# Kernel optimization log

Measured on AMD Instinct MI355X. Metric: run time of the kernel, lower is better.

Reference implementation:

```python
import jax, jax.numpy as jnp
import numpy as np
import math

B, S, D, H = 2048, 32, 1024, 16
DK = D // H
EPS = 1e-5

def setup_inputs() -> dict:
    key = jax.random.key(0)
    ks = jax.random.split(key, 8)
    w_scale = 0.02  # realistic init scale for linear weights
    # Weights stored as (d_in, d_out): y = x @ W + b (same math as torch x @ W.T)
    return {
        "x":  jax.random.normal(ks[0], (B, S, D), jnp.float32),
        "ln_g": jnp.ones((D,), jnp.float32),
        "ln_b": jnp.zeros((D,), jnp.float32),
        "wq": jax.random.normal(ks[1], (D, D), jnp.float32) * w_scale,
        "bq": jnp.zeros((D,), jnp.float32),
        "wk": jax.random.normal(ks[2], (D, D), jnp.float32) * w_scale,
        "bk": jnp.zeros((D,), jnp.float32),
        "wv": jax.random.normal(ks[3], (D, D), jnp.float32) * w_scale,
        "bv": jnp.zeros((D,), jnp.float32),
        "wo": jax.random.normal(ks[4], (D, D), jnp.float32) * w_scale,
        "bo": jnp.zeros((D,), jnp.float32),
        "rel_bias": jax.random.normal(ks[5], (H, 32, 32), jnp.float32),
    }

def reference(x, ln_g, ln_b, wq, bq, wk, bk, wv, bv, wo, bo, rel_bias):
    b, s, d = x.shape
    h = rel_bias.shape[0]
    dk = d // h
    residual = x
    # LayerNorm (eps=1e-5)
    mu = jnp.mean(x, axis=-1, keepdims=True)
    var = jnp.mean(jnp.square(x - mu), axis=-1, keepdims=True)
    xn = (x - mu) * jax.lax.rsqrt(var + EPS) * ln_g + ln_b
    # QKV projections -> [b, h, s, dk]
    def split_heads(t):
        return t.reshape(b, s, h, dk).transpose(0, 2, 1, 3)
    Q = split_heads(xn @ wq + bq)
    K = split_heads(xn @ wk + bk)
    V = split_heads(xn @ wv + bv)
    scores = jnp.einsum('bhqd,bhkd->bhqk', Q, K) / jnp.sqrt(jnp.float32(dk))
    if s <= 32:  # static at trace time, matching the torch branch
        scores = scores + rel_bias[:, :s, :s][None]
    attn = jax.nn.softmax(scores, axis=-1)
    ctx = jnp.einsum('bhqk,bhkd->bhqd', attn, V)
    ctx = ctx.transpose(0, 2, 1, 3).reshape(b, s, d)
    out = ctx @ wo + bo  # dropout is identity in eval
    return residual + out
```

## Files before the change

### kernel.cpp

```cpp
#include <hip/hip_runtime.h>
#include <stdint.h>


typedef __attribute__((ext_vector_type(8))) short bf16x8;
typedef __attribute__((ext_vector_type(4))) float f32x4;
typedef __attribute__((ext_vector_type(16))) float f32x16;

__device__ __forceinline__ float bf2f(unsigned short u) {
    return __uint_as_float(((unsigned)u) << 16);
}
__device__ __forceinline__ unsigned short f2bf(float f) {
    unsigned u = __float_as_uint(f);
    u += 0x7FFFu + ((u >> 16) & 1u);
    return (unsigned short)(u >> 16);
}
__device__ __forceinline__ uint4 pack8(const float* f) {
    uint4 u;
    u.x = (unsigned)f2bf(f[0]) | ((unsigned)f2bf(f[1]) << 16);
    u.y = (unsigned)f2bf(f[2]) | ((unsigned)f2bf(f[3]) << 16);
    u.z = (unsigned)f2bf(f[4]) | ((unsigned)f2bf(f[5]) << 16);
    u.w = (unsigned)f2bf(f[6]) | ((unsigned)f2bf(f[7]) << 16);
    return u;
}

typedef __attribute__((address_space(3))) unsigned lds_u32;
typedef const __attribute__((address_space(1))) unsigned glb_u32;
__device__ __forceinline__ void gld16(const void* g, void* l) {
    __builtin_amdgcn_global_load_lds((glb_u32*)g, (lds_u32*)l, 16, 0, 0);
}

__global__ __launch_bounds__(256) void transpose_w(
    const float* __restrict__ wq, const float* __restrict__ wk,
    const float* __restrict__ wv, const float* __restrict__ wo,
    unsigned short* __restrict__ wcatT, unsigned short* __restrict__ woT)
{
    __shared__ unsigned short T[64 * 72];
    int bid = blockIdx.x;
    int p = bid >> 8;
    int t = bid & 255;
    int k0 = (t >> 4) * 64, n0 = (t & 15) * 64;
    const float* src = (p == 0) ? wq : (p == 1) ? wk : (p == 2) ? wv : wo;
    unsigned short* dst = (p < 3) ? (wcatT + (size_t)p * 1048576) : woT;
    int tid = threadIdx.x;
#pragma unroll
    for (int it = 0; it < 2; it++) {
        int flat = it * 2048 + tid * 8;
        int r = flat >> 6, c = flat & 63;
        const float* s4 = src + (size_t)(k0 + r) * 1024 + n0 + c;
        float4 u0 = *(const float4*)s4;
        float4 u1 = *(const float4*)(s4 + 4);
        float f[8] = {u0.x, u0.y, u0.z, u0.w, u1.x, u1.y, u1.z, u1.w};
        *(uint4*)&T[r * 72 + c] = pack8(f);
    }
    __syncthreads();
#pragma unroll
    for (int it = 0; it < 2; it++) {
        int flat = it * 2048 + tid * 8;
        int rn = flat >> 6, ck = flat & 63;
        unsigned short v[8];
#pragma unroll
        for (int j = 0; j < 8; j++) v[j] = T[(ck + j) * 72 + rn];
        uint4 u;
        u.x = (unsigned)v[0] | ((unsigned)v[1] << 16);
        u.y = (unsigned)v[2] | ((unsigned)v[3] << 16);
        u.z = (unsigned)v[4] | ((unsigned)v[5] << 16);
        u.w = (unsigned)v[6] | ((unsigned)v[7] << 16);
        *(uint4*)(dst + (size_t)(n0 + rn) * 1024 + k0 + ck) = u;
    }
}

__global__ __launch_bounds__(256) void ln_kernel(
    const float* __restrict__ x, const float* __restrict__ gg,
    const float* __restrict__ bb, unsigned short* __restrict__ xn)
{
    int l = threadIdx.x & 63;
    size_t row = (size_t)blockIdx.x * 4 + (threadIdx.x >> 6);
    const float* xr = x + row * 1024;
    float f0[8], f1[8];
    *(float4*)&f0[0] = *(const float4*)(xr + l * 8);
    *(float4*)&f0[4] = *(const float4*)(xr + l * 8 + 4);
    *(float4*)&f1[0] = *(const float4*)(xr + 512 + l * 8);
    *(float4*)&f1[4] = *(const float4*)(xr + 512 + l * 8 + 4);
    float s = 0.f, s2 = 0.f;
#pragma unroll
    for (int j = 0; j < 8; j++) { s += f0[j] + f1[j]; s2 += f0[j] * f0[j] + f1[j] * f1[j]; }
#pragma unroll
    for (int m = 1; m < 64; m <<= 1) { s += __shfl_xor(s, m); s2 += __shfl_xor(s2, m); }
    float mu = s * (1.f / 1024.f);
    float var = s2 * (1.f / 1024.f) - mu * mu;
    float rs = rsqrtf(var + 1e-5f);
    float fg0[8], fg1[8], fb0[8], fb1[8];
    *(float4*)&fg0[0] = *(const float4*)(gg + l * 8);
    *(float4*)&fg0[4] = *(const float4*)(gg + l * 8 + 4);
    *(float4*)&fg1[0] = *(const float4*)(gg + 512 + l * 8);
    *(float4*)&fg1[4] = *(const float4*)(gg + 512 + l * 8 + 4);
    *(float4*)&fb0[0] = *(const float4*)(bb + l * 8);
    *(float4*)&fb0[4] = *(const float4*)(bb + l * 8 + 4);
    *(float4*)&fb1[0] = *(const float4*)(bb + 512 + l * 8);
    *(float4*)&fb1[4] = *(const float4*)(bb + 512 + l * 8 + 4);
    float o0[8], o1[8];
#pragma unroll
    for (int j = 0; j < 8; j++) {
        o0[j] = (f0[j] - mu) * rs * fg0[j] + fb0[j];
        o1[j] = (f1[j] - mu) * rs * fg1[j] + fb1[j];
    }
    *(uint4*)(xn + row * 1024 + l * 8) = pack8(o0);
    *(uint4*)(xn + row * 1024 + 512 + l * 8) = pack8(o1);
}

#define FENCE asm volatile("" ::: "memory")
#define BARRIER do { FENCE; __builtin_amdgcn_s_barrier(); FENCE; } while (0)
#define WAIT_LGKM0 do { asm volatile("s_waitcnt lgkmcnt(0)" ::: "memory"); \
                        __builtin_amdgcn_sched_barrier(0); } while (0)
#define VMCNT(n) asm volatile("s_waitcnt vmcnt(" #n ")" ::: "memory")

#define FQ_SA(buf) (LDSU + (buf) * 16384)
#define FQ_SB(buf) (LDSU + 32768 + (buf) * 12288)
#define QS_OFF 0
#define KS_OFF 18432
#define VT_OFF 36864
#define PS_OFF 57344

#define ASTG(buf, g, koff) gld16(Ag + (size_t)(g) * 65536 + (koff), FQ_SA(buf) + ((g) * 64 + w * 8) * 64)
#define BSTG(buf, p, koff) gld16(((p) == 0 ? Bgq : (p) == 1 ? Bgk : Bgv) + (koff), \
                                 FQ_SB(buf) + ((p) * 64 + w * 8) * 64)

#define FLDA(buf, q, rfq, ks) (*(const bf16x8*)&FQ_SA(buf)[ \
    (wm * 128 + (q) * 32 + (rfq) * 16 + (l & 15)) * 64 + ((((ks) * 32) + khi) ^ aswz)])
#define FLDB(buf, cf, ks) (*(const bf16x8*)&FQ_SB(buf)[ \
    (wn * 48 + (cf) * 16 + (l & 15)) * 64 + ((((ks) * 32) + khi) ^ aswz)])

#define MFMA_TRI(q) do { \
    _Pragma("unroll") \
    for (int cf = 0; cf < 3; cf++) { \
        acc[(q)*2+0][cf] = __builtin_amdgcn_mfma_f32_16x16x32_bf16(aF00, bF[cf][0], acc[(q)*2+0][cf], 0, 0, 0); \
        acc[(q)*2+0][cf] = __builtin_amdgcn_mfma_f32_16x16x32_bf16(aF01, bF[cf][1], acc[(q)*2+0][cf], 0, 0, 0); \
        acc[(q)*2+1][cf] = __builtin_amdgcn_mfma_f32_16x16x32_bf16(aF10, bF[cf][0], acc[(q)*2+1][cf], 0, 0, 0); \
        acc[(q)*2+1][cf] = __builtin_amdgcn_mfma_f32_16x16x32_bf16(aF11, bF[cf][1], acc[(q)*2+1][cf], 0, 0, 0); \
    } } while (0)

#define FPHASE(buf, q, STAGE_STMT, TAIL_STMT) do { \
    bf16x8 aF00 = FLDA(buf, q, 0, 0), aF01 = FLDA(buf, q, 0, 1); \
    bf16x8 aF10 = FLDA(buf, q, 1, 0), aF11 = FLDA(buf, q, 1, 1); \
    if ((q) == 0) { \
        _Pragma("unroll") \
        for (int cf = 0; cf < 3; cf++) { bF[cf][0] = FLDB(buf, cf, 0); bF[cf][1] = FLDB(buf, cf, 1); } \
    } \
    STAGE_STMT; \
    BARRIER; \
    WAIT_LGKM0; \
    __builtin_amdgcn_s_setprio(1); \
    MFMA_TRI(q); \
    __builtin_amdgcn_s_setprio(0); \
    TAIL_STMT; \
    BARRIER; \
} while (0)

__global__ __launch_bounds__(512, 1) void fqa_kernel(
    const unsigned short* __restrict__ A, const unsigned short* __restrict__ wcatT,
    const float* __restrict__ bq, const float* __restrict__ bk,
    const float* __restrict__ bv, const float* __restrict__ rb,
    unsigned short* __restrict__ ctx)
{
    __shared__ __align__(16) unsigned short LDSU[67584];
    int cpx = gridDim.x >> 3;
    int bid = (blockIdx.x & 7) * cpx + (blockIdx.x >> 3);
    int mp = bid >> 4, h = bid & 15;
    int m0 = mp * 256;
    int tid = threadIdx.x, l = tid & 63, w = tid >> 6;
    int wm = w >> 2, wn = w & 3;
    int khi = (l >> 4) * 8;
    int aswz = (l & 7) * 8;
    int swzc = ((l & 7) ^ (l >> 3)) * 8;

    const unsigned short* Ag  = A + (size_t)(m0 + w * 8 + (l >> 3)) * 1024 + swzc;
    const unsigned short* Bgq = wcatT + (size_t)(h * 64 + w * 8 + (l >> 3)) * 1024 + swzc;
    const unsigned short* Bgk = Bgq + 1048576ull;
    const unsigned short* Bgv = Bgq + 2097152ull;

    f32x4 acc[8][3];
#pragma unroll
    for (int i = 0; i < 8; i++)
#pragma unroll
        for (int j = 0; j < 3; j++)
#pragma unroll
            for (int v = 0; v < 4; v++) acc[i][j][v] = 0.f;

    bf16x8 bF[3][2];

    ASTG(0, 0, 0); ASTG(0, 1, 0); ASTG(0, 2, 0); ASTG(0, 3, 0);
    BSTG(0, 0, 0); BSTG(0, 1, 0); BSTG(0, 2, 0);
    BSTG(1, 0, 64); BSTG(1, 1, 64); BSTG(1, 2, 64);
    VMCNT(3);
    BARRIER;

    for (int it = 0; it < 7; ++it) {
        int ko1 = (2 * it + 1) * 64, ko2 = (2 * it + 2) * 64, ko3 = (2 * it + 3) * 64;
        FPHASE(0, 0, do { ASTG(1, 0, ko1); ASTG(1, 1, ko1); } while (0), (void)0);
        FPHASE(0, 1, do { ASTG(1, 2, ko1); ASTG(1, 3, ko1); } while (0), (void)0);
        FPHASE(0, 2, do { BSTG(0, 0, ko2); BSTG(0, 1, ko2); } while (0), (void)0);
        FPHASE(0, 3, BSTG(0, 2, ko2), VMCNT(3));
        FPHASE(1, 0, do { ASTG(0, 0, ko2); ASTG(0, 1, ko2); } while (0), (void)0);
        FPHASE(1, 1, do { ASTG(0, 2, ko2); ASTG(0, 3, ko2); } while (0), (void)0);
        FPHASE(1, 2, do { BSTG(1, 0, ko3); BSTG(1, 1, ko3); } while (0), (void)0);
        FPHASE(1, 3, BSTG(1, 2, ko3), VMCNT(3));
    }
    FPHASE(0, 0, do { ASTG(1, 0, 960); ASTG(1, 1, 960); } while (0), (void)0);
    FPHASE(0, 1, do { ASTG(1, 2, 960); ASTG(1, 3, 960); } while (0), (void)0);
    FPHASE(0, 2, (void)0, (void)0);
    FPHASE(0, 3, (void)0, VMCNT(0));
    FPHASE(1, 0, (void)0, (void)0);
    FPHASE(1, 1, (void)0, (void)0);
    FPHASE(1, 2, (void)0, (void)0);
    FPHASE(1, 3, (void)0, (void)0);
    __builtin_amdgcn_sched_barrier(0);

#pragma unroll
    for (int cf = 0; cf < 3; cf++) {
        int seg = (wn * 3 + cf) >> 2;
        int cseg = wn * 48 + cf * 16 + (l & 15) - (seg << 6);
        const float* bp = (seg == 0) ? bq : (seg == 1) ? bk : bv;
        float bias = bp[h * 64 + cseg];
#pragma unroll
        for (int ai = 0; ai < 8; ai++) {
#pragma unroll
            for (int v = 0; v < 4; v++) {
                int row = wm * 128 + ai * 16 + (l >> 4) * 4 + v;
                unsigned short val = f2bf(acc[ai][cf][v] + bias);
                if (seg == 0)      LDSU[QS_OFF + row * 72 + cseg] = val;
                else if (seg == 1) LDSU[KS_OFF + row * 72 + cseg] = val;
                else               LDSU[VT_OFF + (((row >> 5) << 6) + cseg) * 40 + (row & 31)] = val;
            }
        }
    }
    __syncthreads();

    {
        int col = l & 31, hi = l >> 5;
        f32x16 s;
#pragma unroll
        for (int i = 0; i < 16; i++) s[i] = 0.f;
#pragma unroll
        for (int t = 0; t < 4; t++) {
            bf16x8 aQ = *(const bf16x8*)&LDSU[QS_OFF + (w * 32 + col) * 72 + t * 16 + hi * 8];
            bf16x8 bK = *(const bf16x8*)&LDSU[KS_OFF + (w * 32 + col) * 72 + t * 16 + hi * 8];
            s = __builtin_amdgcn_mfma_f32_32x32x16_bf16(aQ, bK, s, 0, 0, 0);
        }
        const float* rbh = rb + h * 1024;
        unsigned short* ps = LDSU + PS_OFF + w * 1280;
#pragma unroll
        for (int r = 0; r < 16; r++) {
            int m = (r & 3) + 8 * (r >> 2) + 4 * hi;
            float v = s[r] * 0.125f + rbh[m * 32 + col];
            float mx = v;
#pragma unroll
            for (int msk = 1; msk < 32; msk <<= 1) mx = fmaxf(mx, __shfl_xor(mx, msk));
            float e = __expf(v - mx);
            float sm = e;
#pragma unroll
            for (int msk = 1; msk < 32; msk <<= 1) sm += __shfl_xor(sm, msk);
            ps[m * 40 + col] = f2bf(e / sm);
        }
        bf16x8 pa0 = *(const bf16x8*)&ps[col * 40 + hi * 8];
        bf16x8 pa1 = *(const bf16x8*)&ps[col * 40 + 16 + hi * 8];
        size_t rowb = ((size_t)mp * 8 + w) * 32;
#pragma unroll
        for (int c2 = 0; c2 < 2; c2++) {
            bf16x8 vb0 = *(const bf16x8*)&LDSU[VT_OFF + (w * 64 + c2 * 32 + col) * 40 + hi * 8];
            bf16x8 vb1 = *(const bf16x8*)&LDSU[VT_OFF + (w * 64 + c2 * 32 + col) * 40 + 16 + hi * 8];
            f32x16 o;
#pragma unroll
            for (int i = 0; i < 16; i++) o[i] = 0.f;
            o = __builtin_amdgcn_mfma_f32_32x32x16_bf16(pa0, vb0, o, 0, 0, 0);
            o = __builtin_amdgcn_mfma_f32_32x32x16_bf16(pa1, vb1, o, 0, 0, 0);
#pragma unroll
            for (int r = 0; r < 16; r++) {
                int m = (r & 3) + 8 * (r >> 2) + 4 * hi;
                ctx[(rowb + m) * 1024 + h * 64 + c2 * 32 + col] = f2bf(o[r]);
            }
        }
    }
}

#define SAp(buf) (LDSU + (buf) * 16384)
#define SBp(buf) (LDSU + 32768 + (buf) * 16384)

#define STG(gb, hh, kcol, ldsreg) do { \
    const unsigned short* _g = (gb) + (size_t)((hh) * 128) * 1024 + (kcol); \
    unsigned short* _d = (ldsreg) + ((hh) * 128 + w * 8) * 64; \
    gld16(_g, _d); gld16(_g + 64 * 1024, _d + 64 * 64); } while (0)

#define LDA(buf, q, rfq, ks) (*(const bf16x8*)&SAp(buf)[ \
    (wm * 128 + (q) * 32 + (rfq) * 16 + (l & 15)) * 64 + ((((ks) * 32) + khi) ^ aswz)])
#define LDB(buf, cf, ks) (*(const bf16x8*)&SBp(buf)[ \
    (wn * 64 + (cf) * 16 + (l & 15)) * 64 + ((((ks) * 32) + khi) ^ aswz)])

#define MFMA_QUAD(q) do { \
    _Pragma("unroll") \
    for (int cf = 0; cf < 4; cf++) { \
        acc[(q)*2+0][cf] = __builtin_amdgcn_mfma_f32_16x16x32_bf16(aF00, bF[cf][0], acc[(q)*2+0][cf], 0, 0, 0); \
        acc[(q)*2+0][cf] = __builtin_amdgcn_mfma_f32_16x16x32_bf16(aF01, bF[cf][1], acc[(q)*2+0][cf], 0, 0, 0); \
        acc[(q)*2+1][cf] = __builtin_amdgcn_mfma_f32_16x16x32_bf16(aF10, bF[cf][0], acc[(q)*2+1][cf], 0, 0, 0); \
        acc[(q)*2+1][cf] = __builtin_amdgcn_mfma_f32_16x16x32_bf16(aF11, bF[cf][1], acc[(q)*2+1][cf], 0, 0, 0); \
    } } while (0)

#define PHASE(buf, q, STAGE_STMT, TAIL_STMT) do { \
    bf16x8 aF00 = LDA(buf, q, 0, 0), aF01 = LDA(buf, q, 0, 1); \
    bf16x8 aF10 = LDA(buf, q, 1, 0), aF11 = LDA(buf, q, 1, 1); \
    if ((q) == 0) { \
        _Pragma("unroll") \
        for (int cf = 0; cf < 4; cf++) { bF[cf][0] = LDB(buf, cf, 0); bF[cf][1] = LDB(buf, cf, 1); } \
    } \
    STAGE_STMT; \
    BARRIER; \
    WAIT_LGKM0; \
    __builtin_amdgcn_s_setprio(1); \
    MFMA_QUAD(q); \
    __builtin_amdgcn_s_setprio(0); \
    TAIL_STMT; \
    BARRIER; \
} while (0)

__global__ __launch_bounds__(512, 2) void gemm8res(
    const unsigned short* __restrict__ A, const unsigned short* __restrict__ Bt,
    const float* __restrict__ bz0, const float* __restrict__ resid,
    float* __restrict__ out, int NTL)
{
    __shared__ __align__(16) unsigned short LDSU[65536];
    int cpx = gridDim.x >> 3;
    int bid = (blockIdx.x & 7) * cpx + (blockIdx.x >> 3);
    int mt = bid / NTL, ntl = bid % NTL;
    int m0 = mt * 256, n0 = ntl * 256;
    int tid = threadIdx.x, l = tid & 63, w = tid >> 6;
    int wm = w >> 2, wn = w & 3;
    int khi = (l >> 4) * 8;
    int aswz = (l & 7) * 8;

    const unsigned short* Ag = A + (size_t)(m0 + w * 8 + (l >> 3)) * 1024 + ((l & 7) ^ (l >> 3)) * 8;
    const unsigned short* Bg = Bt + (size_t)(n0 + w * 8 + (l >> 3)) * 1024 + ((l & 7) ^ (l >> 3)) * 8;
    unsigned short* sA0 = SAp(0);
    unsigned short* sA1 = SAp(1);
    unsigned short* sB0 = SBp(0);
    unsigned short* sB1 = SBp(1);

    f32x4 acc[8][4];
#pragma unroll
    for (int i = 0; i < 8; i++)
#pragma unroll
        for (int j = 0; j < 4; j++)
#pragma unroll
            for (int v = 0; v < 4; v++) acc[i][j][v] = 0.f;

    bf16x8 bF[4][2];

    STG(Ag, 0, 0, sA0); STG(Ag, 1, 0, sA0);
    STG(Bg, 0, 0, sB0); STG(Bg, 1, 0, sB0);
    STG(Bg, 0, 64, sB1); STG(Bg, 1, 64, sB1);
    VMCNT(4);
    BARRIER;

    for (int it = 0; it < 7; ++it) {
        int koff = it * 128;
        PHASE(0, 0, STG(Ag, 0, koff + 64, sA1), (void)0);
        PHASE(0, 1, STG(Ag, 1, koff + 64, sA1), (void)0);
        PHASE(0, 2, STG(Bg, 0, koff + 128, sB0), (void)0);
        PHASE(0, 3, STG(Bg, 1, koff + 128, sB0), VMCNT(4));
        PHASE(1, 0, STG(Ag, 0, koff + 128, sA0), (void)0);
        PHASE(1, 1, STG(Ag, 1, koff + 128, sA0), (void)0);
        PHASE(1, 2, STG(Bg, 0, koff + 192, sB1), (void)0);
        PHASE(1, 3, STG(Bg, 1, koff + 192, sB1), VMCNT(4));
    }
    PHASE(0, 0, STG(Ag, 0, 960, sA1), (void)0);
    PHASE(0, 1, STG(Ag, 1, 960, sA1), (void)0);
    PHASE(0, 2, (void)0, (void)0);
    PHASE(0, 3, (void)0, VMCNT(0));
    PHASE(1, 0, (void)0, (void)0);
    PHASE(1, 1, (void)0, (void)0);
    PHASE(1, 2, (void)0, (void)0);
    PHASE(1, 3, (void)0, (void)0);
    __builtin_amdgcn_sched_barrier(0);

    float* Cf = (float*)LDSU;
    int gcol = n0 + l * 4;
    float4 bzv = *(const float4*)(bz0 + gcol);
#pragma unroll
    for (int pass = 0; pass < 2; pass++) {
        __syncthreads();
#pragma unroll
        for (int rfq = 0; rfq < 4; rfq++) {
            int rf = pass * 4 + rfq;
#pragma unroll
            for (int cf = 0; cf < 4; cf++) {
                int c0 = wn * 64 + cf * 16 + (l & 15);
                int c4 = c0 >> 2, ce = c0 & 3;
#pragma unroll
                for (int v = 0; v < 4; v++) {
                    int rl = wm * 64 + rfq * 16 + (l >> 4) * 4 + v;
                    Cf[rl * 256 + ((c4 ^ (rl & 7)) << 2) + ce] = acc[rf][cf][v];
                }
            }
        }
        __syncthreads();
#pragma unroll
        for (int rb4 = 0; rb4 < 4; rb4++) {
            float4 rz[4], cv[4];
#pragma unroll
            for (int k = 0; k < 4; k++) {
                int rr = (rb4 * 4 + k) * 8 + w;
                int grow = m0 + (rr & 63) + ((rr >> 6) << 7) + pass * 64;
                rz[k] = *(const float4*)(resid + (size_t)grow * 1024 + gcol);
            }
#pragma unroll
            for (int k = 0; k < 4; k++) {
                int rr = (rb4 * 4 + k) * 8 + w;
                cv[k] = *(const float4*)&Cf[rr * 256 + ((l ^ (rr & 7)) << 2)];
            }
#pragma unroll
            for (int k = 0; k < 4; k++) {
                int rr = (rb4 * 4 + k) * 8 + w;
                int grow = m0 + (rr & 63) + ((rr >> 6) << 7) + pass * 64;
                float4 o;
                o.x = cv[k].x + bzv.x + rz[k].x;
                o.y = cv[k].y + bzv.y + rz[k].y;
                o.z = cv[k].z + bzv.z + rz[k].z;
                o.w = cv[k].w + bzv.w + rz[k].w;
                *(float4*)(out + (size_t)grow * 1024 + gcol) = o;
            }
        }
    }
}

extern "C" void kernel_launch(void* const* d_in, const int* in_sizes, int n_in,
                              void* d_out, int out_size, void* d_ws, size_t ws_size,
                              hipStream_t stream)
{
    const float* x  = (const float*)d_in[0];
    const float* lg = (const float*)d_in[1];
    const float* lb = (const float*)d_in[2];
    const float* wq = (const float*)d_in[3];
    const float* bq = (const float*)d_in[4];
    const float* wk = (const float*)d_in[5];
    const float* bk = (const float*)d_in[6];
    const float* wv = (const float*)d_in[7];
    const float* bv = (const float*)d_in[8];
    const float* wo = (const float*)d_in[9];
    const float* bo = (const float*)d_in[10];
    const float* rb = (const float*)d_in[11];
    float* out = (float*)d_out;
    unsigned short* ws = (unsigned short*)d_ws;

    unsigned short* wcatT = ws;
    unsigned short* woT   = wcatT + 3145728;
    unsigned short* xn    = woT + 1048576;
    unsigned short* ctx   = xn + 67108864ull;

    transpose_w<<<dim3(1024), dim3(256), 0, stream>>>(wq, wk, wv, wo, wcatT, woT);
    ln_kernel<<<dim3(16384), dim3(256), 0, stream>>>(x, lg, lb, xn);

    fqa_kernel<<<dim3(4096), dim3(512), 0, stream>>>(xn, wcatT, bq, bk, bv, rb, ctx);

    gemm8res<<<dim3(1024), dim3(512), 0, stream>>>(ctx, woT, bo, x, out, 4);
}
```

Baseline: 782.1 us.

## Halve fused QKV-attention tile to 128 rows with 256-thread blocks, two per CU

The fused LN-output x QKV projection plus attention kernel now processes 128 rows per block with 4 waves instead of 256 rows with 8 waves. Each wave computes a 64x96 tile with six column fragments, and LDS drops to about 80KB so two blocks can be resident per CU. The grid doubles to 8192 blocks. The aim is better latency hiding and occupancy, at the cost of reading the weight tiles from global memory twice as often per output row.

After: 777.8 us. About the same (-0.5%).

```diff
diff --git a/kernel.cpp b/kernel.cpp
--- a/kernel.cpp
+++ b/kernel.cpp
@@ -114,61 +114,59 @@
                         __builtin_amdgcn_sched_barrier(0); } while (0)
 #define VMCNT(n) asm volatile("s_waitcnt vmcnt(" #n ")" ::: "memory")
 
-#define FQ_SA(buf) (LDSU + (buf) * 16384)
-#define FQ_SB(buf) (LDSU + 32768 + (buf) * 12288)
+#define FQ_SA(buf) (LDSU + (buf) * 8192)
+#define FQ_SB(buf) (LDSU + 16384 + (buf) * 12288)
 #define QS_OFF 0
-#define KS_OFF 18432
-#define VT_OFF 36864
-#define PS_OFF 57344
-
-#define ASTG(buf, g, koff) gld16(Ag + (size_t)(g) * 65536 + (koff), FQ_SA(buf) + ((g) * 64 + w * 8) * 64)
-#define BSTG(buf, p, koff) gld16(((p) == 0 ? Bgq : (p) == 1 ? Bgk : Bgv) + (koff), \
-                                 FQ_SB(buf) + ((p) * 64 + w * 8) * 64)
-
-#define FLDA(buf, q, rfq, ks) (*(const bf16x8*)&FQ_SA(buf)[ \
-    (wm * 128 + (q) * 32 + (rfq) * 16 + (l & 15)) * 64 + ((((ks) * 32) + khi) ^ aswz)])
+#define KS_OFF 9216
+#define VT_OFF 18432
+#define PS_OFF 28672
+
+#define ASTG(buf, g, koff) gld16(Ag + (size_t)(g) * 32768 + (koff), \
+                                 FQ_SA(buf) + ((g) * 32 + w * 8) * 64)
+#define BSTG(buf, p, c, koff) gld16(((p) == 0 ? Bgq : (p) == 1 ? Bgk : Bgv) + (size_t)(c) * 32768 + (koff), \
+                                    FQ_SB(buf) + ((p) * 64 + (c) * 32 + w * 8) * 64)
+
+#define FLDA(buf, q, ks) (*(const bf16x8*)&FQ_SA(buf)[ \
+    (wm * 64 + (q) * 16 + (l & 15)) * 64 + ((((ks) * 32) + khi) ^ aswz)])
 #define FLDB(buf, cf, ks) (*(const bf16x8*)&FQ_SB(buf)[ \
-    (wn * 48 + (cf) * 16 + (l & 15)) * 64 + ((((ks) * 32) + khi) ^ aswz)])
-
-#define MFMA_TRI(q) do { \
+    (wn * 96 + (cf) * 16 + (l & 15)) * 64 + ((((ks) * 32) + khi) ^ aswz)])
+
+#define MFMA_HEX(q) do { \
     _Pragma("unroll") \
-    for (int cf = 0; cf < 3; cf++) { \
-        acc[(q)*2+0][cf] = __builtin_amdgcn_mfma_f32_16x16x32_bf16(aF00, bF[cf][0], acc[(q)*2+0][cf], 0, 0, 0); \
-        acc[(q)*2+0][cf] = __builtin_amdgcn_mfma_f32_16x16x32_bf16(aF01, bF[cf][1], acc[(q)*2+0][cf], 0, 0, 0); \
-        acc[(q)*2+1][cf] = __builtin_amdgcn_mfma_f32_16x16x32_bf16(aF10, bF[cf][0], acc[(q)*2+1][cf], 0, 0, 0); \
-        acc[(q)*2+1][cf] = __builtin_amdgcn_mfma_f32_16x16x32_bf16(aF11, bF[cf][1], acc[(q)*2+1][cf], 0, 0, 0); \
+    for (int cf = 0; cf < 6; cf++) { \
+        acc[q][cf] = __builtin_amdgcn_mfma_f32_16x16x32_bf16(aF0, bF[cf][0], acc[q][cf], 0, 0, 0); \
+        acc[q][cf] = __builtin_amdgcn_mfma_f32_16x16x32_bf16(aF1, bF[cf][1], acc[q][cf], 0, 0, 0); \
     } } while (0)
 
 #define FPHASE(buf, q, STAGE_STMT, TAIL_STMT) do { \
-    bf16x8 aF00 = FLDA(buf, q, 0, 0), aF01 = FLDA(buf, q, 0, 1); \
-    bf16x8 aF10 = FLDA(buf, q, 1, 0), aF11 = FLDA(buf, q, 1, 1); \
+    bf16x8 aF0 = FLDA(buf, q, 0), aF1 = FLDA(buf, q, 1); \
     if ((q) == 0) { \
         _Pragma("unroll") \
-        for (int cf = 0; cf < 3; cf++) { bF[cf][0] = FLDB(buf, cf, 0); bF[cf][1] = FLDB(buf, cf, 1); } \
+        for (int cf = 0; cf < 6; cf++) { bF[cf][0] = FLDB(buf, cf, 0); bF[cf][1] = FLDB(buf, cf, 1); } \
     } \
     STAGE_STMT; \
     BARRIER; \
     WAIT_LGKM0; \
     __builtin_amdgcn_s_setprio(1); \
-    MFMA_TRI(q); \
+    MFMA_HEX(q); \
     __builtin_amdgcn_s_setprio(0); \
     TAIL_STMT; \
     BARRIER; \
 } while (0)
 
-__global__ __launch_bounds__(512, 1) void fqa_kernel(
+__global__ __launch_bounds__(256, 2) void fqa2_kernel(
     const unsigned short* __restrict__ A, const unsigned short* __restrict__ wcatT,
     const float* __restrict__ bq, const float* __restrict__ bk,
     const float* __restrict__ bv, const float* __restrict__ rb,
     unsigned short* __restrict__ ctx)
 {
-    __shared__ __align__(16) unsigned short LDSU[67584];
+    __shared__ __align__(16) unsigned short LDSU[40960];
     int cpx = gridDim.x >> 3;
     int bid = (blockIdx.x & 7) * cpx + (blockIdx.x >> 3);
     int mp = bid >> 4, h = bid & 15;
-    int m0 = mp * 256;
+    int m0 = mp * 128;
     int tid = threadIdx.x, l = tid & 63, w = tid >> 6;
-    int wm = w >> 2, wn = w & 3;
+    int wm = w >> 1, wn = w & 1;
     int khi = (l >> 4) * 8;
     int aswz = (l & 7) * 8;
     int swzc = ((l & 7) ^ (l >> 3)) * 8;
@@ -178,32 +176,34 @@
     const unsigned short* Bgk = Bgq + 1048576ull;
     const unsigned short* Bgv = Bgq + 2097152ull;
 
-    f32x4 acc[8][3];
-#pragma unroll
-    for (int i = 0; i < 8; i++)
-#pragma unroll
-        for (int j = 0; j < 3; j++)
+    f32x4 acc[4][6];
+#pragma unroll
+    for (int i = 0; i < 4; i++)
+#pragma unroll
+        for (int j = 0; j < 6; j++)
 #pragma unroll
             for (int v = 0; v < 4; v++) acc[i][j][v] = 0.f;
 
-    bf16x8 bF[3][2];
+    bf16x8 bF[6][2];
 
     ASTG(0, 0, 0); ASTG(0, 1, 0); ASTG(0, 2, 0); ASTG(0, 3, 0);
-    BSTG(0, 0, 0); BSTG(0, 1, 0); BSTG(0, 2, 0);
-    BSTG(1, 0, 64); BSTG(1, 1, 64); BSTG(1, 2, 64);
-    VMCNT(3);
+    BSTG(0, 0, 0, 0); BSTG(0, 0, 1, 0); BSTG(0, 1, 0, 0);
+    BSTG(0, 1, 1, 0); BSTG(0, 2, 0, 0); BSTG(0, 2, 1, 0);
+    BSTG(1, 0, 0, 64); BSTG(1, 0, 1, 64); BSTG(1, 1, 0, 64);
+    BSTG(1, 1, 1, 64); BSTG(1, 2, 0, 64); BSTG(1, 2, 1, 64);
+    VMCNT(6);
     BARRIER;
 
     for (int it = 0; it < 7; ++it) {
         int ko1 = (2 * it + 1) * 64, ko2 = (2 * it + 2) * 64, ko3 = (2 * it + 3) * 64;
         FPHASE(0, 0, do { ASTG(1, 0, ko1); ASTG(1, 1, ko1); } while (0), (void)0);
         FPHASE(0, 1, do { ASTG(1, 2, ko1); ASTG(1, 3, ko1); } while (0), (void)0);
-        FPHASE(0, 2, do { BSTG(0, 0, ko2); BSTG(0, 1, ko2); } while (0), (void)0);
-        FPHASE(0, 3, BSTG(0, 2, ko2), VMCNT(3));
+        FPHASE(0, 2, do { BSTG(0, 0, 0, ko2); BSTG(0, 0, 1, ko2); BSTG(0, 1, 0, ko2); } while (0), (void)0);
+        FPHASE(0, 3, do { BSTG(0, 1, 1, ko2); BSTG(0, 2, 0, ko2); BSTG(0, 2, 1, ko2); } while (0), VMCNT(6));
         FPHASE(1, 0, do { ASTG(0, 0, ko2); ASTG(0, 1, ko2); } while (0), (void)0);
         FPHASE(1, 1, do { ASTG(0, 2, ko2); ASTG(0, 3, ko2); } while (0), (void)0);
-        FPHASE(1, 2, do { BSTG(1, 0, ko3); BSTG(1, 1, ko3); } while (0), (void)0);
-        FPHASE(1, 3, BSTG(1, 2, ko3), VMCNT(3));
+        FPHASE(1, 2, do { BSTG(1, 0, 0, ko3); BSTG(1, 0, 1, ko3); BSTG(1, 1, 0, ko3); } while (0), (void)0);
+        FPHASE(1, 3, do { BSTG(1, 1, 1, ko3); BSTG(1, 2, 0, ko3); BSTG(1, 2, 1, ko3); } while (0), VMCNT(6));
     }
     FPHASE(0, 0, do { ASTG(1, 0, 960); ASTG(1, 1, 960); } while (0), (void)0);
     FPHASE(0, 1, do { ASTG(1, 2, 960); ASTG(1, 3, 960); } while (0), (void)0);
@@ -216,16 +216,17 @@
     __builtin_amdgcn_sched_barrier(0);
 
 #pragma unroll
-    for (int cf = 0; cf < 3; cf++) {
-        int seg = (wn * 3 + cf) >> 2;
-        int cseg = wn * 48 + cf * 16 + (l & 15) - (seg << 6);
+    for (int cf = 0; cf < 6; cf++) {
+        int colg = wn * 96 + cf * 16 + (l & 15);
+        int seg = colg >> 6;
+        int cseg = colg & 63;
         const float* bp = (seg == 0) ? bq : (seg == 1) ? bk : bv;
         float bias = bp[h * 64 + cseg];
 #pragma unroll
-        for (int ai = 0; ai < 8; ai++) {
+        for (int ai = 0; ai < 4; ai++) {
 #pragma unroll
             for (int v = 0; v < 4; v++) {
-                int row = wm * 128 + ai * 16 + (l >> 4) * 4 + v;
+                int row = wm * 64 + ai * 16 + (l >> 4) * 4 + v;
                 unsigned short val = f2bf(acc[ai][cf][v] + bias);
                 if (seg == 0)      LDSU[QS_OFF + row * 72 + cseg] = val;
                 else if (seg == 1) LDSU[KS_OFF + row * 72 + cseg] = val;
@@ -263,7 +264,7 @@
         }
         bf16x8 pa0 = *(const bf16x8*)&ps[col * 40 + hi * 8];
         bf16x8 pa1 = *(const bf16x8*)&ps[col * 40 + 16 + hi * 8];
-        size_t rowb = ((size_t)mp * 8 + w) * 32;
+        size_t rowb = ((size_t)mp * 4 + w) * 32;
 #pragma unroll
         for (int c2 = 0; c2 < 2; c2++) {
             bf16x8 vb0 = *(const bf16x8*)&LDSU[VT_OFF + (w * 64 + c2 * 32 + col) * 40 + hi * 8];
@@ -282,8 +283,8 @@
     }
 }
 
-#define SAp(buf) (LDSU + (buf) * 16384)
-#define SBp(buf) (LDSU + 32768 + (buf) * 16384)
+#define SAp(buf) (LDSB + (buf) * 16384)
+#define SBp(buf) (LDSB + 32768 + (buf) * 16384)
 
 #define STG(gb, hh, kcol, ldsreg) do { \
     const unsigned short* _g = (gb) + (size_t)((hh) * 128) * 1024 + (kcol); \
@@ -326,7 +327,7 @@
     const float* __restrict__ bz0, const float* __restrict__ resid,
     float* __restrict__ out, int NTL)
 {
-    __shared__ __align__(16) unsigned short LDSU[65536];
+    __shared__ __align__(16) unsigned short LDSB[65536];
     int cpx = gridDim.x >> 3;
     int bid = (blockIdx.x & 7) * cpx + (blockIdx.x >> 3);
     int mt = bid / NTL, ntl = bid % NTL;
@@ -380,7 +381,7 @@
     PHASE(1, 3, (void)0, (void)0);
     __builtin_amdgcn_sched_barrier(0);
 
-    float* Cf = (float*)LDSU;
+    float* Cf = (float*)LDSB;
     int gcol = n0 + l * 4;
     float4 bzv = *(const float4*)(bz0 + gcol);
 #pragma unroll
@@ -457,7 +458,7 @@
     transpose_w<<<dim3(1024), dim3(256), 0, stream>>>(wq, wk, wv, wo, wcatT, woT);
     ln_kernel<<<dim3(16384), dim3(256), 0, stream>>>(x, lg, lb, xn);
 
-    fqa_kernel<<<dim3(4096), dim3(512), 0, stream>>>(xn, wcatT, bq, bk, bv, rb, ctx);
+    fqa2_kernel<<<dim3(8192), dim3(256), 0, stream>>>(xn, wcatT, bq, bk, bv, rb, ctx);
 
     gemm8res<<<dim3(1024), dim3(512), 0, stream>>>(ctx, woT, bo, x, out, 4);
 }
```
